# Performance work log

Hardware: AMD Instinct MI355X
Metric: run time of the kernel (lower is better)

The kernel has to match this reference:

```python
import math
import jax, jax.numpy as jnp
import numpy as np

N = 50000      # num nodes
E = 400000     # num edges
IN = 128       # in_channels
HID = 64       # hidden_channels
HEADS = 4
OUT = 32       # out_channels
TDIM = 16      # time_dim
NEG_SLOPE = 0.2
EPS = 1e-5


def setup_inputs() -> dict:
    key = jax.random.key(0)
    ks = jax.random.split(key, 20)
    s = 0.05
    # Fourier time encoder: Linear(1, TDIM) with freq-pattern weight
    freq = np.exp(np.arange(0, TDIM, 2, dtype=np.float32) * -(math.log(10000.0) / TDIM))
    tw = np.zeros((TDIM,), dtype=np.float32)
    tw[0::2] = freq
    tw[1::2] = freq
    return {
        "x": jax.random.normal(ks[0], (N, IN), jnp.float32),
        "edge_index": jax.random.randint(ks[1], (2, E), 0, N, jnp.int64),
        "edge_time": jax.random.uniform(ks[2], (E,), jnp.float32),
        "time_w": jnp.asarray(tw),
        "time_b": jax.random.normal(ks[3], (TDIM,), jnp.float32) * s,
        "proj_w": jax.random.normal(ks[4], (IN + TDIM, IN), jnp.float32) * s,
        "proj_b": jax.random.normal(ks[5], (IN,), jnp.float32) * s,
        "W1": jax.random.normal(ks[6], (IN, HEADS * HID), jnp.float32) * s,
        "a_src1": jax.random.normal(ks[7], (HEADS, HID), jnp.float32) * s,
        "a_dst1": jax.random.normal(ks[8], (HEADS, HID), jnp.float32) * s,
        "b1": jax.random.normal(ks[9], (HEADS * HID,), jnp.float32) * s,
        "g1": jnp.ones((HEADS * HID,), jnp.float32),
        "be1": jnp.zeros((HEADS * HID,), jnp.float32),
        "W2": jax.random.normal(ks[10], (HEADS * HID, OUT), jnp.float32) * s,
        "a_src2": jax.random.normal(ks[11], (1, OUT), jnp.float32) * s,
        "a_dst2": jax.random.normal(ks[12], (1, OUT), jnp.float32) * s,
        "b2": jax.random.normal(ks[13], (OUT,), jnp.float32) * s,
        "g2": jnp.ones((OUT,), jnp.float32),
        "be2": jnp.zeros((OUT,), jnp.float32),
    }


def layer_norm(h, g, b):
    mu = jnp.mean(h, axis=-1, keepdims=True)
    var = jnp.mean(jnp.square(h - mu), axis=-1, keepdims=True)
    return (h - mu) * jax.lax.rsqrt(var + EPS) * g + b


def gat_conv(x, src, dst, W, a_src, a_dst, bias, heads, ch, concat):
    """PyG GATConv (self-loops pre-appended in src/dst), inference (no dropout)."""
    n = x.shape[0]
    h = (x @ W).reshape(n, heads, ch)                       # [N,H,C]
    al_s = jnp.sum(h * a_src, axis=-1)                      # [N,H]
    al_d = jnp.sum(h * a_dst, axis=-1)                      # [N,H]
    e = al_s[src] + al_d[dst]                               # [Etot,H]
    e = jnp.where(e > 0, e, NEG_SLOPE * e)                  # leaky_relu
    m = jax.ops.segment_max(e, dst, num_segments=n)         # scatter-softmax
    ex = jnp.exp(e - m[dst])
    denom = jax.ops.segment_sum(ex, dst, num_segments=n)
    alpha = ex / denom[dst]                                 # [Etot,H]
    out = jax.ops.segment_sum(h[src] * alpha[:, :, None], dst, num_segments=n)  # [N,H,C]
    out = out.reshape(n, heads * ch) if concat else jnp.mean(out, axis=1)
    return out + bias


def reference(x, edge_index, edge_time, time_w, time_b, proj_w, proj_b,
              W1, a_src1, a_dst1, b1, g1, be1,
              W2, a_src2, a_dst2, b2, g2, be2):
    src, dst = edge_index[0], edge_index[1]
    # Fourier time encoding of edge timestamps
    tp = edge_time[:, None] * time_w + time_b               # [E,TDIM]
    even = (jnp.arange(TDIM) % 2) == 0
    t_enc = jnp.where(even, jnp.sin(tp), jnp.cos(tp))       # [E,TDIM]
    # scatter_reduce_(mean, include_self=True) onto source nodes: sum/(count+1)
    t_sum = jax.ops.segment_sum(t_enc, src, num_segments=N)
    cnt = jax.ops.segment_sum(jnp.ones((E,), x.dtype), src, num_segments=N)
    node_time = t_sum / (cnt + 1.0)[:, None]
    xin = jnp.concatenate([x, node_time], axis=-1) @ proj_w + proj_b  # [N,IN]
    # add self loops (PyG GATConv default)
    loop = jnp.arange(N, dtype=src.dtype)
    src2 = jnp.concatenate([src, loop])
    dst2 = jnp.concatenate([dst, loop])
    h = gat_conv(xin, src2, dst2, W1, a_src1, a_dst1, b1, HEADS, HID, True)
    h = jax.nn.elu(h)
    h = layer_norm(h, g1, be1)
    h = gat_conv(h, src2, dst2, W2, a_src2, a_dst2, b2, 1, OUT, False)
    h = layer_norm(h, g2, be2)
    return h
```

## Files before the change

### kernel.cpp

```cpp
#include <hip/hip_runtime.h>
#include <math.h>

#define NN 50000
#define EE 400000
#define INC 128
#define TD 16
#define H1C 256
#define OUTC 32
#define NEG 0.2f
#define PAD 64
#define DSTRIDE 32

#define EB 391
#define WB 168
#define PB 782

typedef _Float16 f16;
typedef __attribute__((ext_vector_type(8))) _Float16 f16x8;
typedef __attribute__((ext_vector_type(2))) _Float16 f16x2;
typedef __attribute__((ext_vector_type(4))) float f32x4;

__device__ __forceinline__ float leaky(float x) { return x > 0.f ? x : NEG * x; }
__device__ __forceinline__ float sel4f(const float4& v, int h) {
  return h == 0 ? v.x : h == 1 ? v.y : h == 2 ? v.z : v.w;
}

__global__ __launch_bounds__(256) void k_rank_proj(
    const int* __restrict__ ei, const float* __restrict__ et,
    int* __restrict__ deg_dst, int* __restrict__ deg_src,
    int* __restrict__ src_pad, float* __restrict__ et_pad,
    const float* __restrict__ W1, const float* __restrict__ W2,
    f16* __restrict__ W1T, f16* __restrict__ W2T, f16* __restrict__ pwtT,
    const float* __restrict__ x, const float* __restrict__ pw,
    const float* __restrict__ pb, f16* __restrict__ xin) {
  __shared__ f16 A[64 * 136];
  int tid = threadIdx.x;
  int b = blockIdx.x;
  if (b < EB) {
    int gid = b * 256 + tid;
    if (gid < EE / 4) {
      int4 sv = *(const int4*)(ei + gid * 4);
      int4 dv = *(const int4*)(ei + EE + gid * 4);
      float4 tv = *(const float4*)(et + gid * 4);
      int rd0 = atomicAdd(&deg_dst[dv.x * DSTRIDE], 1);
      int rd1 = atomicAdd(&deg_dst[dv.y * DSTRIDE], 1);
      int rd2 = atomicAdd(&deg_dst[dv.z * DSTRIDE], 1);
      int rd3 = atomicAdd(&deg_dst[dv.w * DSTRIDE], 1);
      int rs0 = atomicAdd(&deg_src[sv.x * DSTRIDE], 1);
      int rs1 = atomicAdd(&deg_src[sv.y * DSTRIDE], 1);
      int rs2 = atomicAdd(&deg_src[sv.z * DSTRIDE], 1);
      int rs3 = atomicAdd(&deg_src[sv.w * DSTRIDE], 1);
      if (rd0 < PAD) src_pad[dv.x * PAD + rd0] = sv.x;
      if (rd1 < PAD) src_pad[dv.y * PAD + rd1] = sv.y;
      if (rd2 < PAD) src_pad[dv.z * PAD + rd2] = sv.z;
      if (rd3 < PAD) src_pad[dv.w * PAD + rd3] = sv.w;
      if (rs0 < PAD) et_pad[sv.x * PAD + rs0] = tv.x;
      if (rs1 < PAD) et_pad[sv.y * PAD + rs1] = tv.y;
      if (rs2 < PAD) et_pad[sv.z * PAD + rs2] = tv.z;
      if (rs3 < PAD) et_pad[sv.w * PAD + rs3] = tv.w;
    }
    return;
  }
  if (b < EB + WB) {
    int idx = (b - EB) * 256 + tid;
    if (idx < 32768) {
      int c = idx >> 7, k = idx & 127;
      W1T[idx] = (f16)W1[k * 256 + c];
    } else if (idx < 40960) {
      int i3 = idx - 32768;
      int c = i3 >> 8, k = i3 & 255;
      W2T[i3] = (f16)W2[k * 32 + c];
    } else if (idx < 43008) {
      int i4 = idx - 40960;
      pwtT[i4] = (f16)pw[16384 + i4];
    }
    return;
  }
  int n0 = (b - EB - WB) * 64;
  int l = tid & 63, w = tid >> 6;
  for (int ci = tid; ci < 1024; ci += 256) {
    int r = ci >> 4, c8 = (ci & 15) * 8;
    int n = n0 + r;
    f16x8 hv = {};
    if (n < NN) {
      float4 v0 = *(const float4*)(x + (size_t)n * INC + c8);
      float4 v1 = *(const float4*)(x + (size_t)n * INC + c8 + 4);
      hv[0] = (f16)v0.x; hv[1] = (f16)v0.y; hv[2] = (f16)v0.z; hv[3] = (f16)v0.w;
      hv[4] = (f16)v1.x; hv[5] = (f16)v1.y; hv[6] = (f16)v1.z; hv[7] = (f16)v1.w;
    }
    *(f16x8*)(A + r * 136 + c8) = hv;
  }
  int r16 = l & 15, g = l >> 4;
  f16x8 breg[2][4];
  #pragma unroll
  for (int jj = 0; jj < 2; ++jj) {
    int col = w * 32 + jj * 16 + r16;
    #pragma unroll
    for (int kk = 0; kk < 4; ++kk)
      #pragma unroll
      for (int t = 0; t < 8; ++t)
        breg[jj][kk][t] = (f16)pw[(size_t)(kk * 32 + g * 8 + t) * 128 + col];
  }
  f32x4 acc[4][2];
  #pragma unroll
  for (int i = 0; i < 4; ++i)
    #pragma unroll
    for (int jj = 0; jj < 2; ++jj) acc[i][jj] = (f32x4){0.f, 0.f, 0.f, 0.f};
  __syncthreads();
  #pragma unroll
  for (int kk = 0; kk < 4; ++kk)
    #pragma unroll
    for (int i = 0; i < 4; ++i) {
      f16x8 a = *(const f16x8*)(A + (i * 16 + r16) * 136 + kk * 32 + g * 8);
      acc[i][0] = __builtin_amdgcn_mfma_f32_16x16x32_f16(a, breg[0][kk], acc[i][0], 0, 0, 0);
      acc[i][1] = __builtin_amdgcn_mfma_f32_16x16x32_f16(a, breg[1][kk], acc[i][1], 0, 0, 0);
    }
  #pragma unroll
  for (int i = 0; i < 4; ++i)
    #pragma unroll
    for (int jj = 0; jj < 2; ++jj) {
      int col = w * 32 + jj * 16 + r16;
      float bj = pb[col];
      #pragma unroll
      for (int q = 0; q < 4; ++q) {
        int row = n0 + i * 16 + g * 4 + q;
        if (row < NN) xin[(size_t)row * INC + col] = (f16)(acc[i][jj][q] + bj);
      }
    }
}

__global__ __launch_bounds__(256) void k_h1t(
    const f16* __restrict__ xin, const f16* __restrict__ W1T,
    const float* __restrict__ as1, const float* __restrict__ ad1,
    const int* __restrict__ deg_src, const float* __restrict__ et_pad,
    const float* __restrict__ tw, const float* __restrict__ tb,
    const f16* __restrict__ pwtT, f16* __restrict__ h1,
    float* __restrict__ als, float* __restrict__ ald) {
  __shared__ f16 A[64 * 136];
  __shared__ f16 pwl[16 * 128];
  __shared__ float nt[64][16];
  int tid = threadIdx.x, l = tid & 63, w = tid >> 6;
  int n0 = blockIdx.x * 64;
  for (int i = tid; i < 2048; i += 256)
    pwl[i] = pwtT[i];
  {
    int r = tid >> 2, kq = (tid & 3) * 4;
    int n = n0 + r;
    int cnt = (n < NN) ? min(deg_src[n * DSTRIDE], PAD) : 0;
    float w0 = tw[kq], w1 = tw[kq + 1], w2 = tw[kq + 2], w3 = tw[kq + 3];
    float b0 = tb[kq], b1 = tb[kq + 1], b2 = tb[kq + 2], b3 = tb[kq + 3];
    float v0 = 0.f, v1 = 0.f, v2 = 0.f, v3 = 0.f;
    const float* ep = et_pad + (size_t)n * PAD;
    for (int i = 0; i < cnt; ++i) {
      float e = ep[i];
      v0 += __sinf(fmaf(e, w0, b0));
      v1 += __cosf(fmaf(e, w1, b1));
      v2 += __sinf(fmaf(e, w2, b2));
      v3 += __cosf(fmaf(e, w3, b3));
    }
    float inv = 1.f / (float)(cnt + 1);
    nt[r][kq] = v0 * inv; nt[r][kq + 1] = v1 * inv;
    nt[r][kq + 2] = v2 * inv; nt[r][kq + 3] = v3 * inv;
  }
  __syncthreads();
  f16x8 zero = {};
  for (int ci = tid; ci < 1024; ci += 256) {
    int r = ci >> 4, c8 = (ci & 15) * 8;
    int n = n0 + r;
    f16x8 v = (n < NN) ? *(const f16x8*)(xin + (size_t)n * INC + c8) : zero;
    float av[8];
    #pragma unroll
    for (int u = 0; u < 8; ++u) av[u] = (float)v[u];
    #pragma unroll
    for (int t = 0; t < 16; ++t) {
      float ntv = nt[r][t];
      f16x8 pv = *(const f16x8*)(pwl + t * 128 + c8);
      #pragma unroll
      for (int u = 0; u < 8; ++u) av[u] = fmaf(ntv, (float)pv[u], av[u]);
    }
    f16x8 ov;
    #pragma unroll
    for (int u = 0; u < 8; ++u) ov[u] = (f16)av[u];
    *(f16x8*)(A + r * 136 + c8) = ov;
  }
  int r16 = l & 15, g = l >> 4;
  f16x8 breg[4][4];
  #pragma unroll
  for (int jj = 0; jj < 4; ++jj) {
    int col = w * 64 + jj * 16 + r16;
    #pragma unroll
    for (int kk = 0; kk < 4; ++kk)
      breg[jj][kk] = *(const f16x8*)(W1T + col * 128 + kk * 32 + g * 8);
  }
  f32x4 acc[4][4];
  #pragma unroll
  for (int i = 0; i < 4; ++i)
    #pragma unroll
    for (int jj = 0; jj < 4; ++jj) acc[i][jj] = (f32x4){0.f, 0.f, 0.f, 0.f};
  __syncthreads();
  #pragma unroll
  for (int kk = 0; kk < 4; ++kk)
    #pragma unroll
    for (int i = 0; i < 4; ++i) {
      f16x8 a = *(const f16x8*)(A + (i * 16 + r16) * 136 + kk * 32 + g * 8);
      #pragma unroll
      for (int jj = 0; jj < 4; ++jj)
        acc[i][jj] = __builtin_amdgcn_mfma_f32_16x16x32_f16(a, breg[jj][kk], acc[i][jj], 0, 0, 0);
    }
  #pragma unroll
  for (int i = 0; i < 4; ++i)
    #pragma unroll
    for (int jj = 0; jj < 4; ++jj) {
      int col = w * 64 + jj * 16 + r16;
      #pragma unroll
      for (int q = 0; q < 4; ++q) {
        int row = n0 + i * 16 + g * 4 + q;
        if (row < NN) h1[(size_t)row * H1C + col] = (f16)acc[i][jj][q];
      }
    }
  float asc[4], adc[4];
  #pragma unroll
  for (int jj = 0; jj < 4; ++jj) {
    int col = w * 64 + jj * 16 + r16;
    asc[jj] = as1[col];
    adc[jj] = ad1[col];
  }
  #pragma unroll
  for (int i = 0; i < 4; ++i)
    #pragma unroll
    for (int q = 0; q < 4; ++q) {
      float ps = 0.f, pd = 0.f;
      #pragma unroll
      for (int jj = 0; jj < 4; ++jj) {
        ps = fmaf(acc[i][jj][q], asc[jj], ps);
        pd = fmaf(acc[i][jj][q], adc[jj], pd);
      }
      #pragma unroll
      for (int o = 1; o < 16; o <<= 1) {
        ps += __shfl_xor(ps, o);
        pd += __shfl_xor(pd, o);
      }
      int row = n0 + i * 16 + g * 4 + q;
      if (r16 == 0 && row < NN) {
        als[row * 4 + w] = ps;
        ald[row * 4 + w] = pd;
      }
    }
}

__global__ __launch_bounds__(256) void k_h2g(const f16* __restrict__ ln1,
                                             const f16* __restrict__ W2T,
                                             const float* __restrict__ as2,
                                             const float* __restrict__ ad2,
                                             f16* __restrict__ h2,
                                             float* __restrict__ als2,
                                             float* __restrict__ ald2) {
  __shared__ f16 A[64 * 264];
  int tid = threadIdx.x, l = tid & 63, w = tid >> 6;
  int n0 = blockIdx.x * 64;
  f16x8 zero = {};
  for (int ci = tid; ci < 2048; ci += 256) {
    int r = ci >> 5, c8 = (ci & 31) * 8;
    int n = n0 + r;
    f16x8 v = (n < NN) ? *(const f16x8*)(ln1 + (size_t)n * H1C + c8) : zero;
    *(f16x8*)(A + r * 264 + c8) = v;
  }
  int r16 = l & 15, g = l >> 4;
  f16x8 breg[2][8];
  #pragma unroll
  for (int jj = 0; jj < 2; ++jj) {
    int col = jj * 16 + r16;
    #pragma unroll
    for (int kk = 0; kk < 8; ++kk)
      breg[jj][kk] = *(const f16x8*)(W2T + col * 256 + kk * 32 + g * 8);
  }
  f32x4 acc[2];
  acc[0] = (f32x4){0.f, 0.f, 0.f, 0.f};
  acc[1] = (f32x4){0.f, 0.f, 0.f, 0.f};
  __syncthreads();
  #pragma unroll
  for (int kk = 0; kk < 8; ++kk) {
    f16x8 a = *(const f16x8*)(A + (w * 16 + r16) * 264 + kk * 32 + g * 8);
    acc[0] = __builtin_amdgcn_mfma_f32_16x16x32_f16(a, breg[0][kk], acc[0], 0, 0, 0);
    acc[1] = __builtin_amdgcn_mfma_f32_16x16x32_f16(a, breg[1][kk], acc[1], 0, 0, 0);
  }
  #pragma unroll
  for (int jj = 0; jj < 2; ++jj)
    #pragma unroll
    for (int q = 0; q < 4; ++q) {
      int row = n0 + w * 16 + g * 4 + q;
      int col = jj * 16 + r16;
      if (row < NN) h2[(size_t)row * OUTC + col] = (f16)acc[jj][q];
    }
  float as_0 = as2[r16], as_1 = as2[16 + r16];
  float ad_0 = ad2[r16], ad_1 = ad2[16 + r16];
  #pragma unroll
  for (int q = 0; q < 4; ++q) {
    float ps = acc[0][q] * as_0 + acc[1][q] * as_1;
    float pd = acc[0][q] * ad_0 + acc[1][q] * ad_1;
    #pragma unroll
    for (int o = 1; o < 16; o <<= 1) {
      ps += __shfl_xor(ps, o);
      pd += __shfl_xor(pd, o);
    }
    int row = n0 + w * 16 + g * 4 + q;
    if (r16 == 0 && row < NN) {
      als2[row] = ps;
      ald2[row] = pd;
    }
  }
}

__global__ __launch_bounds__(256) void k_agg1(
    const int* __restrict__ deg_dst, const int* __restrict__ src_pad,
    const f16* __restrict__ h1, const float* __restrict__ als,
    const float* __restrict__ ald, const float* __restrict__ b1,
    const float* __restrict__ g1, const float* __restrict__ be1,
    f16* __restrict__ ln1) {
  __shared__ int s_s[8][32];
  __shared__ float s_e[8][128];
  int tid = threadIdx.x;
  int grp = tid >> 5, l32 = tid & 31;
  int n = blockIdx.x * 8 + grp;
  int cnt = min(deg_dst[n * DSTRIDE], PAD);
  const int* sp = src_pad + (size_t)n * PAD;
  const float4 adv = *(const float4*)(ald + n * 4);
  int hh = l32 >> 3;
  int c0 = l32 * 8;
  float adh = sel4f(adv, hh);
  float seh = __expf(leaky(als[n * 4 + hh] + adh));

  f16x2 accA[4] = {}, accB[4] = {}, accC[4] = {}, accD[4] = {};
  float d = 0.f;
  for (int base = 0; base < cnt; base += 32) {
    int p = base + l32;
    if (p < cnt) {
      int sv = sp[p];
      const float4 a = *(const float4*)(als + sv * 4);
      float4 e4;
      e4.x = __expf(leaky(a.x + adv.x));
      e4.y = __expf(leaky(a.y + adv.y));
      e4.z = __expf(leaky(a.z + adv.z));
      e4.w = __expf(leaky(a.w + adv.w));
      s_s[grp][l32] = sv;
      *(float4*)(&s_e[grp][l32 * 4]) = e4;
    }
    int lim = cnt - base;
    if (lim > 32) lim = 32;
    int j = 0;
    for (; j + 4 <= lim; j += 4) {
      int sA = s_s[grp][j], sB = s_s[grp][j + 1];
      int sC = s_s[grp][j + 2], sD = s_s[grp][j + 3];
      float aA = s_e[grp][j * 4 + hh], aB = s_e[grp][(j + 1) * 4 + hh];
      float aC = s_e[grp][(j + 2) * 4 + hh], aD = s_e[grp][(j + 3) * 4 + hh];
      f16x8 hA = *(const f16x8*)(h1 + (size_t)sA * H1C + c0);
      f16x8 hB = *(const f16x8*)(h1 + (size_t)sB * H1C + c0);
      f16x8 hC = *(const f16x8*)(h1 + (size_t)sC * H1C + c0);
      f16x8 hD = *(const f16x8*)(h1 + (size_t)sD * H1C + c0);
      f16 tA = (f16)aA, tB = (f16)aB, tC = (f16)aC, tD = (f16)aD;
      f16x2 vA = {tA, tA}, vB = {tB, tB}, vC = {tC, tC}, vD = {tD, tD};
      const f16x2* pA = (const f16x2*)&hA;
      const f16x2* pB = (const f16x2*)&hB;
      const f16x2* pC = (const f16x2*)&hC;
      const f16x2* pD = (const f16x2*)&hD;
      #pragma unroll
      for (int k = 0; k < 4; ++k) {
        accA[k] = pA[k] * vA + accA[k];
        accB[k] = pB[k] * vB + accB[k];
        accC[k] = pC[k] * vC + accC[k];
        accD[k] = pD[k] * vD + accD[k];
      }
      d += (aA + aB) + (aC + aD);
    }
    for (; j + 2 <= lim; j += 2) {
      int sA = s_s[grp][j], sB = s_s[grp][j + 1];
      float aA = s_e[grp][j * 4 + hh], aB = s_e[grp][(j + 1) * 4 + hh];
      f16x8 hA = *(const f16x8*)(h1 + (size_t)sA * H1C + c0);
      f16x8 hB = *(const f16x8*)(h1 + (size_t)sB * H1C + c0);
      f16 tA = (f16)aA, tB = (f16)aB;
      f16x2 vA = {tA, tA}, vB = {tB, tB};
      const f16x2* pA = (const f16x2*)&hA;
      const f16x2* pB = (const f16x2*)&hB;
      #pragma unroll
      for (int k = 0; k < 4; ++k) {
        accA[k] = pA[k] * vA + accA[k];
        accB[k] = pB[k] * vB + accB[k];
      }
      d += aA + aB;
    }
    if (j < lim) {
      int sA = s_s[grp][j];
      float aA = s_e[grp][j * 4 + hh];
      f16x8 hA = *(const f16x8*)(h1 + (size_t)sA * H1C + c0);
      f16 tA = (f16)aA;
      f16x2 vA = {tA, tA};
      const f16x2* pA = (const f16x2*)&hA;
      #pragma unroll
      for (int k = 0; k < 4; ++k) accA[k] = pA[k] * vA + accA[k];
      d += aA;
    }
  }
  d += seh;
  float invd = __builtin_amdgcn_rcpf(d);
  f16x8 hv = *(const f16x8*)(h1 + (size_t)n * H1C + c0);
  const f16* fa = (const f16*)accA;
  const f16* fb = (const f16*)accB;
  const f16* fc = (const f16*)accC;
  const f16* fd = (const f16*)accD;
  float4 ba = *(const float4*)(b1 + c0), bb = *(const float4*)(b1 + c0 + 4);
  float v[8];
  #pragma unroll
  for (int u = 0; u < 8; ++u) {
    float bu = u < 4 ? (&ba.x)[u] : (&bb.x)[u - 4];
    float sum = ((float)fa[u] + (float)fb[u]) + ((float)fc[u] + (float)fd[u]);
    float t = fmaf((float)hv[u], seh, sum);
    t = fmaf(t, invd, bu);
    v[u] = t > 0.f ? t : (__expf(t) - 1.f);
  }
  float s1 = 0.f, s2 = 0.f;
  #pragma unroll
  for (int u = 0; u < 8; ++u) { s1 += v[u]; s2 += v[u] * v[u]; }
  #pragma unroll
  for (int o = 16; o >= 1; o >>= 1) {
    s1 += __shfl_xor(s1, o, 32);
    s2 += __shfl_xor(s2, o, 32);
  }
  float mu = s1 * (1.f / 256.f);
  float var = s2 * (1.f / 256.f) - mu * mu;
  float sc = rsqrtf(var + 1e-5f);
  float4 ga = *(const float4*)(g1 + c0), gb = *(const float4*)(g1 + c0 + 4);
  float4 ea = *(const float4*)(be1 + c0), eb = *(const float4*)(be1 + c0 + 4);
  f16x8 o8;
  #pragma unroll
  for (int u = 0; u < 8; ++u) {
    float gu = u < 4 ? (&ga.x)[u] : (&gb.x)[u - 4];
    float eu = u < 4 ? (&ea.x)[u] : (&eb.x)[u - 4];
    o8[u] = (f16)((v[u] - mu) * sc * gu + eu);
  }
  *(f16x8*)(ln1 + (size_t)n * H1C + c0) = o8;
}

__global__ __launch_bounds__(256) void k_agg2(
    const int* __restrict__ deg_dst, const int* __restrict__ src_pad,
    const f16* __restrict__ h2, const float* __restrict__ als2,
    const float* __restrict__ ald2, const float* __restrict__ b2,
    const float* __restrict__ g2, const float* __restrict__ be2,
    float* __restrict__ out) {
  int tid = threadIdx.x;
  int n = blockIdx.x * 8 + (tid >> 5);
  int ch = tid & 31;
  int cnt = min(deg_dst[n * DSTRIDE], PAD);
  const int* sp = src_pad + (size_t)n * PAD;
  float adn = ald2[n];
  float se = __expf(leaky(als2[n] + adn));
  float acc0 = (float)h2[(size_t)n * OUTC + ch] * se;
  float acc1 = 0.f, acc2 = 0.f, acc3 = 0.f;
  float d0 = se, d1 = 0.f, d2 = 0.f, d3 = 0.f;
  int i = 0;
  for (; i + 4 <= cnt; i += 4) {
    int s0 = sp[i], s1v = sp[i + 1], s2v = sp[i + 2], s3v = sp[i + 3];
    float e0 = __expf(leaky(als2[s0] + adn));
    float e1 = __expf(leaky(als2[s1v] + adn));
    float e2 = __expf(leaky(als2[s2v] + adn));
    float e3 = __expf(leaky(als2[s3v] + adn));
    acc0 = fmaf((float)h2[(size_t)s0 * OUTC + ch], e0, acc0);
    acc1 = fmaf((float)h2[(size_t)s1v * OUTC + ch], e1, acc1);
    acc2 = fmaf((float)h2[(size_t)s2v * OUTC + ch], e2, acc2);
    acc3 = fmaf((float)h2[(size_t)s3v * OUTC + ch], e3, acc3);
    d0 += e0; d1 += e1; d2 += e2; d3 += e3;
  }
  for (; i < cnt; ++i) {
    int s0 = sp[i];
    float e0 = __expf(leaky(als2[s0] + adn));
    acc0 = fmaf((float)h2[(size_t)s0 * OUTC + ch], e0, acc0);
    d0 += e0;
  }
  float invd = __builtin_amdgcn_rcpf((d0 + d1) + (d2 + d3));
  float t = fmaf((acc0 + acc1) + (acc2 + acc3), invd, b2[ch]);
  float s1 = t, s2 = t * t;
  #pragma unroll
  for (int o = 16; o >= 1; o >>= 1) {
    s1 += __shfl_xor(s1, o, 32);
    s2 += __shfl_xor(s2, o, 32);
  }
  float mu = s1 * (1.f / 32.f);
  float var = s2 * (1.f / 32.f) - mu * mu;
  float sc = rsqrtf(var + 1e-5f);
  out[(size_t)n * OUTC + ch] = (t - mu) * sc * g2[ch] + be2[ch];
}

extern "C" void kernel_launch(void* const* d_in, const int* in_sizes, int n_in,
                              void* d_out, int out_size, void* d_ws, size_t ws_size,
                              hipStream_t stream) {
  const float* x   = (const float*)d_in[0];
  const int*   ei  = (const int*)d_in[1];
  const float* et  = (const float*)d_in[2];
  const float* tw  = (const float*)d_in[3];
  const float* tb  = (const float*)d_in[4];
  const float* pw  = (const float*)d_in[5];
  const float* pb  = (const float*)d_in[6];
  const float* W1  = (const float*)d_in[7];
  const float* as1 = (const float*)d_in[8];
  const float* ad1 = (const float*)d_in[9];
  const float* b1  = (const float*)d_in[10];
  const float* g1  = (const float*)d_in[11];
  const float* be1 = (const float*)d_in[12];
  const float* W2  = (const float*)d_in[13];
  const float* as2 = (const float*)d_in[14];
  const float* ad2 = (const float*)d_in[15];
  const float* b2  = (const float*)d_in[16];
  const float* g2  = (const float*)d_in[17];
  const float* be2 = (const float*)d_in[18];

  char* ws = (char*)d_ws;
  size_t off = 0;
  auto alloc = [&](size_t bytes) {
    void* p = ws + off;
    off += (bytes + 255) & ~(size_t)255;
    return p;
  };
  f16* xin   = (f16*)alloc((size_t)NN * INC * 2);
  f16* h1    = (f16*)alloc((size_t)NN * H1C * 2);
  f16* ln1   = (f16*)alloc((size_t)NN * H1C * 2);
  f16* h2    = (f16*)alloc((size_t)NN * OUTC * 2);
  float* als1v = (float*)alloc((size_t)NN * 4 * 4);
  float* ald1v = (float*)alloc((size_t)NN * 4 * 4);
  float* als2v = (float*)alloc((size_t)NN * 4);
  float* ald2v = (float*)alloc((size_t)NN * 4);
  int*   src_pad = (int*)alloc((size_t)NN * PAD * 4);
  float* et_pad  = (float*)alloc((size_t)NN * PAD * 4);
  f16* W1T = (f16*)alloc(32768 * 2);
  f16* W2T = (f16*)alloc(8192 * 2);
  f16* pwtT = (f16*)alloc(2048 * 2);
  int* deg_dst = (int*)alloc((size_t)NN * DSTRIDE * 4);
  int* deg_src = (int*)alloc((size_t)NN * DSTRIDE * 4);

  hipMemsetAsync(deg_dst, 0, (size_t)NN * DSTRIDE * 4, stream);
  hipMemsetAsync(deg_src, 0, (size_t)NN * DSTRIDE * 4, stream);

  const int NT64 = (NN + 63) / 64;
  k_rank_proj<<<EB + WB + PB, 256, 0, stream>>>(ei, et, deg_dst, deg_src, src_pad,
                                                et_pad, W1, W2, W1T, W2T, pwtT,
                                                x, pw, pb, xin);
  k_h1t<<<NT64, 256, 0, stream>>>(xin, W1T, as1, ad1, deg_src, et_pad, tw, tb, pwtT,
                                  h1, als1v, ald1v);
  k_agg1<<<NN / 8, 256, 0, stream>>>(deg_dst, src_pad, h1, als1v, ald1v,
                                     b1, g1, be1, ln1);
  k_h2g<<<NT64, 256, 0, stream>>>(ln1, W2T, as2, ad2, h2, als2v, ald2v);
  k_agg2<<<NN / 8, 256, 0, stream>>>(deg_dst, src_pad, h2, als2v, ald2v,
                                     b2, g2, be2, (float*)d_out);
}
```

Baseline: 164.4 us.

## Pack degree counters densely, merge memsets, process eight edges per thread

Removes the 32-int stride padding on the per-node degree counters, so each counter now sits in a dense array instead of its own 128-byte slot. Both counters share one allocation cleared by a single memset, which makes the two memsets (about 12.8 MB total) much smaller. Each edge-ranking thread now handles eight edges instead of four, halving the block count. The risk is more atomic contention and false sharing on cache lines that now hold several nodes' counters, and less parallelism in the edge phase.

```diff
diff --git a/kernel.cpp b/kernel.cpp
--- a/kernel.cpp
+++ b/kernel.cpp
@@ -9,9 +9,8 @@
 #define OUTC 32
 #define NEG 0.2f
 #define PAD 64
-#define DSTRIDE 32
-
-#define EB 391
+
+#define EB 196
 #define WB 168
 #define PB 782
 
@@ -38,26 +37,46 @@
   int b = blockIdx.x;
   if (b < EB) {
     int gid = b * 256 + tid;
-    if (gid < EE / 4) {
-      int4 sv = *(const int4*)(ei + gid * 4);
-      int4 dv = *(const int4*)(ei + EE + gid * 4);
-      float4 tv = *(const float4*)(et + gid * 4);
-      int rd0 = atomicAdd(&deg_dst[dv.x * DSTRIDE], 1);
-      int rd1 = atomicAdd(&deg_dst[dv.y * DSTRIDE], 1);
-      int rd2 = atomicAdd(&deg_dst[dv.z * DSTRIDE], 1);
-      int rd3 = atomicAdd(&deg_dst[dv.w * DSTRIDE], 1);
-      int rs0 = atomicAdd(&deg_src[sv.x * DSTRIDE], 1);
-      int rs1 = atomicAdd(&deg_src[sv.y * DSTRIDE], 1);
-      int rs2 = atomicAdd(&deg_src[sv.z * DSTRIDE], 1);
-      int rs3 = atomicAdd(&deg_src[sv.w * DSTRIDE], 1);
-      if (rd0 < PAD) src_pad[dv.x * PAD + rd0] = sv.x;
-      if (rd1 < PAD) src_pad[dv.y * PAD + rd1] = sv.y;
-      if (rd2 < PAD) src_pad[dv.z * PAD + rd2] = sv.z;
-      if (rd3 < PAD) src_pad[dv.w * PAD + rd3] = sv.w;
-      if (rs0 < PAD) et_pad[sv.x * PAD + rs0] = tv.x;
-      if (rs1 < PAD) et_pad[sv.y * PAD + rs1] = tv.y;
-      if (rs2 < PAD) et_pad[sv.z * PAD + rs2] = tv.z;
-      if (rs3 < PAD) et_pad[sv.w * PAD + rs3] = tv.w;
+    if (gid < EE / 8) {
+      int e0 = gid * 8;
+      int4 sva = *(const int4*)(ei + e0);
+      int4 svb = *(const int4*)(ei + e0 + 4);
+      int4 dva = *(const int4*)(ei + EE + e0);
+      int4 dvb = *(const int4*)(ei + EE + e0 + 4);
+      float4 tva = *(const float4*)(et + e0);
+      float4 tvb = *(const float4*)(et + e0 + 4);
+      int rd0 = atomicAdd(&deg_dst[dva.x], 1);
+      int rd1 = atomicAdd(&deg_dst[dva.y], 1);
+      int rd2 = atomicAdd(&deg_dst[dva.z], 1);
+      int rd3 = atomicAdd(&deg_dst[dva.w], 1);
+      int rd4 = atomicAdd(&deg_dst[dvb.x], 1);
+      int rd5 = atomicAdd(&deg_dst[dvb.y], 1);
+      int rd6 = atomicAdd(&deg_dst[dvb.z], 1);
+      int rd7 = atomicAdd(&deg_dst[dvb.w], 1);
+      int rs0 = atomicAdd(&deg_src[sva.x], 1);
+      int rs1 = atomicAdd(&deg_src[sva.y], 1);
+      int rs2 = atomicAdd(&deg_src[sva.z], 1);
+      int rs3 = atomicAdd(&deg_src[sva.w], 1);
+      int rs4 = atomicAdd(&deg_src[svb.x], 1);
+      int rs5 = atomicAdd(&deg_src[svb.y], 1);
+      int rs6 = atomicAdd(&deg_src[svb.z], 1);
+      int rs7 = atomicAdd(&deg_src[svb.w], 1);
+      if (rd0 < PAD) src_pad[dva.x * PAD + rd0] = sva.x;
+      if (rd1 < PAD) src_pad[dva.y * PAD + rd1] = sva.y;
+      if (rd2 < PAD) src_pad[dva.z * PAD + rd2] = sva.z;
+      if (rd3 < PAD) src_pad[dva.w * PAD + rd3] = sva.w;
+      if (rd4 < PAD) src_pad[dvb.x * PAD + rd4] = svb.x;
+      if (rd5 < PAD) src_pad[dvb.y * PAD + rd5] = svb.y;
+      if (rd6 < PAD) src_pad[dvb.z * PAD + rd6] = svb.z;
+      if (rd7 < PAD) src_pad[dvb.w * PAD + rd7] = svb.w;
+      if (rs0 < PAD) et_pad[sva.x * PAD + rs0] = tva.x;
+      if (rs1 < PAD) et_pad[sva.y * PAD + rs1] = tva.y;
+      if (rs2 < PAD) et_pad[sva.z * PAD + rs2] = tva.z;
+      if (rs3 < PAD) et_pad[sva.w * PAD + rs3] = tva.w;
+      if (rs4 < PAD) et_pad[svb.x * PAD + rs4] = tvb.x;
+      if (rs5 < PAD) et_pad[svb.y * PAD + rs5] = tvb.y;
+      if (rs6 < PAD) et_pad[svb.z * PAD + rs6] = tvb.z;
+      if (rs7 < PAD) et_pad[svb.w * PAD + rs7] = tvb.w;
     }
     return;
   }
@@ -146,7 +165,7 @@
   {
     int r = tid >> 2, kq = (tid & 3) * 4;
     int n = n0 + r;
-    int cnt = (n < NN) ? min(deg_src[n * DSTRIDE], PAD) : 0;
+    int cnt = (n < NN) ? min(deg_src[n], PAD) : 0;
     float w0 = tw[kq], w1 = tw[kq + 1], w2 = tw[kq + 2], w3 = tw[kq + 3];
     float b0 = tb[kq], b1 = tb[kq + 1], b2 = tb[kq + 2], b3 = tb[kq + 3];
     float v0 = 0.f, v1 = 0.f, v2 = 0.f, v3 = 0.f;
@@ -322,7 +341,7 @@
   int tid = threadIdx.x;
   int grp = tid >> 5, l32 = tid & 31;
   int n = blockIdx.x * 8 + grp;
-  int cnt = min(deg_dst[n * DSTRIDE], PAD);
+  int cnt = min(deg_dst[n], PAD);
   const int* sp = src_pad + (size_t)n * PAD;
   const float4 adv = *(const float4*)(ald + n * 4);
   int hh = l32 >> 3;
@@ -449,7 +468,7 @@
   int tid = threadIdx.x;
   int n = blockIdx.x * 8 + (tid >> 5);
   int ch = tid & 31;
-  int cnt = min(deg_dst[n * DSTRIDE], PAD);
+  int cnt = min(deg_dst[n], PAD);
   const int* sp = src_pad + (size_t)n * PAD;
   float adn = ald2[n];
   float se = __expf(leaky(als2[n] + adn));
@@ -532,11 +551,11 @@
   f16* W1T = (f16*)alloc(32768 * 2);
   f16* W2T = (f16*)alloc(8192 * 2);
   f16* pwtT = (f16*)alloc(2048 * 2);
-  int* deg_dst = (int*)alloc((size_t)NN * DSTRIDE * 4);
-  int* deg_src = (int*)alloc((size_t)NN * DSTRIDE * 4);
-
-  hipMemsetAsync(deg_dst, 0, (size_t)NN * DSTRIDE * 4, stream);
-  hipMemsetAsync(deg_src, 0, (size_t)NN * DSTRIDE * 4, stream);
+  int* deg2 = (int*)alloc((size_t)NN * 2 * 4);
+  int* deg_dst = deg2;
+  int* deg_src = deg2 + NN;
+
+  hipMemsetAsync(deg2, 0, (size_t)NN * 2 * 4, stream);
 
   const int NT64 = (NN + 63) / 64;
   k_rank_proj<<<EB + WB + PB, 256, 0, stream>>>(ei, et, deg_dst, deg_src, src_pad,
```

New measurement: 161.4 us. Within noise of the previous version (-1.8%).
